# Kernel optimization log

Measured on AMD Instinct MI355X. Metric: run time of the kernel, lower is better.

## Reference

```python
import jax, jax.numpy as jnp
import numpy as np

N = 131072   # octree nodes at this depth
C = 192      # channels (depthwise)
K = 27       # 3x3x3 neighbor stencil
BN_EPS = 1e-5


def setup_inputs() -> dict:
    key = jax.random.key(0)
    k1, k2, k3 = jax.random.split(key, 3)
    data = jax.random.normal(k1, (N, C), dtype=jnp.float32)
    # Octree neighbor table: for each node, indices of its 27 stencil neighbors.
    neigh = jax.random.randint(k2, (N, K), 0, N)
    # Depthwise weights [K, C] (OctreeDWConv, use_bias=False)
    weight = jax.random.normal(k3, (K, C), dtype=jnp.float32) * 0.05
    gamma = jnp.ones((C,), dtype=jnp.float32)
    beta = jnp.zeros((C,), dtype=jnp.float32)
    return {"data": data, "neigh": neigh, "weight": weight,
            "gamma": gamma, "beta": beta}


def reference(data, neigh, weight, gamma, beta):
    # Depthwise octree conv: out[n, c] = sum_k data[neigh[n, k], c] * weight[k, c]
    # Scan over the 27 stencil taps so we never materialize the [N, K, C] gather.
    def step(acc, kin):
        idx_k, w_k = kin          # idx_k: [N], w_k: [C]
        return acc + data[idx_k] * w_k, None

    acc0 = jnp.zeros_like(data)
    out, _ = jax.lax.scan(step, acc0, (neigh.T, weight))  # out: [N, C]

    # BatchNorm1d (training mode: batch statistics over the node dimension)
    mean = jnp.mean(out, axis=0)
    var = jnp.var(out, axis=0)
    return (out - mean) * jax.lax.rsqrt(var + BN_EPS) * gamma + beta
```

## Files before the change

### kernel.cpp

```cpp
#include <hip/hip_runtime.h>


static constexpr int NN = 131072;
static constexpr int CC = 192;
static constexpr int KK = 27;
static constexpr int NB = 32;
static constexpr float BN_EPS = 1e-5f;

typedef float          f32x4 __attribute__((ext_vector_type(4)));
typedef unsigned short u16x4 __attribute__((ext_vector_type(4)));
typedef unsigned int   u32x2 __attribute__((ext_vector_type(2)));

__device__ __forceinline__ unsigned short f2bf_rne(float x) {
    unsigned u = __float_as_uint(x);
    return (unsigned short)((u + 0x7FFFu + ((u >> 16) & 1u)) >> 16);
}

__global__ __launch_bounds__(256) void cvt_zero(
    const float* __restrict__ src, unsigned short* __restrict__ dst,
    float* __restrict__ stats )
{
    if (blockIdx.x < 2 && threadIdx.x < CC)
        stats[blockIdx.x * CC + threadIdx.x] = 0.f;

    const int i = blockIdx.x * 256 + threadIdx.x;
    const f32x4 v =
        __builtin_nontemporal_load(reinterpret_cast<const f32x4*>(src) + i);
    u16x4 o;
    o.x = f2bf_rne(v.x); o.y = f2bf_rne(v.y);
    o.z = f2bf_rne(v.z); o.w = f2bf_rne(v.w);
    reinterpret_cast<u16x4*>(dst)[i] = o;
}

__global__ __launch_bounds__(192, 8) void conv_r4(
    const unsigned short* __restrict__ data_bf,
    const int*   __restrict__ neigh,
    const float* __restrict__ weight,
    unsigned short* __restrict__ conv_bf,
    float*       __restrict__ ch_sum,
    float*       __restrict__ ch_sumsq)
{
    __shared__ float lds_w[KK * CC];

    const int c    = threadIdx.x;
    const int base = blockIdx.x * NB;

#pragma unroll
    for (int k = 0; k < KK; ++k) lds_w[k * CC + c] = weight[k * CC + c];
    __syncthreads();

    float s = 0.f, ss = 0.f;

    for (int n = 0; n < NB; ++n) {
        const int node = base + n;
        const int* nrow = neigh + node * KK;

        unsigned short r[KK];
#pragma unroll
        for (int k = 0; k < KK; ++k)
            r[k] = data_bf[(size_t)nrow[k] * CC + c];

        float acc = 0.f;
#pragma unroll
        for (int k = 0; k < KK; ++k)
            acc = fmaf(__uint_as_float((unsigned)r[k] << 16),
                       lds_w[k * CC + c], acc);

        __builtin_nontemporal_store(f2bf_rne(acc),
                                    &conv_bf[(size_t)node * CC + c]);
        s  += acc;
        ss += acc * acc;
    }

    atomicAdd(&ch_sum[c],   s);
    atomicAdd(&ch_sumsq[c], ss);
}

__global__ __launch_bounds__(192) void bn_apply_fused(
    const unsigned int* __restrict__ conv_bf,
    const float* __restrict__ ch_sum,
    const float* __restrict__ ch_sumsq,
    const float* __restrict__ gamma,
    const float* __restrict__ beta,
    float* __restrict__ out)
{
    const int t = threadIdx.x;
    const int g = t / 48;
    const int q = t - g * 48;
    const int cb = q * 4;

    const float inv_n = 1.0f / (float)NN;
    f32x4 sc, bi;
    {
        float m0 = ch_sum[cb + 0] * inv_n, m1 = ch_sum[cb + 1] * inv_n;
        float m2 = ch_sum[cb + 2] * inv_n, m3 = ch_sum[cb + 3] * inv_n;
        float v0 = ch_sumsq[cb + 0] * inv_n - m0 * m0;
        float v1 = ch_sumsq[cb + 1] * inv_n - m1 * m1;
        float v2 = ch_sumsq[cb + 2] * inv_n - m2 * m2;
        float v3 = ch_sumsq[cb + 3] * inv_n - m3 * m3;
        sc.x = gamma[cb + 0] * rsqrtf(v0 + BN_EPS);
        sc.y = gamma[cb + 1] * rsqrtf(v1 + BN_EPS);
        sc.z = gamma[cb + 2] * rsqrtf(v2 + BN_EPS);
        sc.w = gamma[cb + 3] * rsqrtf(v3 + BN_EPS);
        bi.x = beta[cb + 0] - m0 * sc.x;
        bi.y = beta[cb + 1] - m1 * sc.y;
        bi.z = beta[cb + 2] - m2 * sc.z;
        bi.w = beta[cb + 3] - m3 * sc.w;
    }

    for (int nb = blockIdx.x; nb < NN / 4; nb += gridDim.x) {
        const int node = nb * 4 + g;
        const int i = node * 48 + q;
        const u32x2 u = __builtin_nontemporal_load(
            reinterpret_cast<const u32x2*>(conv_bf) + i);
        f32x4 v;
        v.x = fmaf(__uint_as_float(u.x << 16),         sc.x, bi.x);
        v.y = fmaf(__uint_as_float(u.x & 0xFFFF0000u), sc.y, bi.y);
        v.z = fmaf(__uint_as_float(u.y << 16),         sc.z, bi.z);
        v.w = fmaf(__uint_as_float(u.y & 0xFFFF0000u), sc.w, bi.w);
        __builtin_nontemporal_store(v, reinterpret_cast<f32x4*>(out) + i);
    }
}

__global__ __launch_bounds__(CC) void conv_bn_partial_f32(
    const float* __restrict__ data,
    const int*   __restrict__ neigh,
    const float* __restrict__ weight,
    float*       __restrict__ conv_out,
    float*       __restrict__ ch_sum,
    float*       __restrict__ ch_sumsq)
{
    const int c = threadIdx.x;
    const int base = blockIdx.x * NB;
    float w[KK];
#pragma unroll
    for (int k = 0; k < KK; ++k) w[k] = weight[k * CC + c];
    float s = 0.f, ss = 0.f;
    for (int n = 0; n < NB; ++n) {
        const int node = base + n;
        const int* nrow = neigh + node * KK;
        float acc = 0.f;
#pragma unroll
        for (int k = 0; k < KK; ++k)
            acc = fmaf(data[nrow[k] * CC + c], w[k], acc);
        conv_out[node * CC + c] = acc;
        s += acc; ss += acc * acc;
    }
    atomicAdd(&ch_sum[c], s);
    atomicAdd(&ch_sumsq[c], ss);
}

__global__ __launch_bounds__(192) void bn_apply_f32_fused(
    float* __restrict__ out,
    const float* __restrict__ ch_sum,
    const float* __restrict__ ch_sumsq,
    const float* __restrict__ gamma,
    const float* __restrict__ beta)
{
    const int t = threadIdx.x;
    const int g = t / 48;
    const int q = t - g * 48;
    const int cb = q * 4;
    const float inv_n = 1.0f / (float)NN;
    float4 sc, bi;
    float m0 = ch_sum[cb+0]*inv_n, m1 = ch_sum[cb+1]*inv_n;
    float m2 = ch_sum[cb+2]*inv_n, m3 = ch_sum[cb+3]*inv_n;
    sc.x = gamma[cb+0]*rsqrtf(ch_sumsq[cb+0]*inv_n - m0*m0 + BN_EPS);
    sc.y = gamma[cb+1]*rsqrtf(ch_sumsq[cb+1]*inv_n - m1*m1 + BN_EPS);
    sc.z = gamma[cb+2]*rsqrtf(ch_sumsq[cb+2]*inv_n - m2*m2 + BN_EPS);
    sc.w = gamma[cb+3]*rsqrtf(ch_sumsq[cb+3]*inv_n - m3*m3 + BN_EPS);
    bi.x = beta[cb+0] - m0*sc.x; bi.y = beta[cb+1] - m1*sc.y;
    bi.z = beta[cb+2] - m2*sc.z; bi.w = beta[cb+3] - m3*sc.w;
    for (int nb = blockIdx.x; nb < NN / 4; nb += gridDim.x) {
        const int i = (nb * 4 + g) * 48 + q;
        float4 v = reinterpret_cast<float4*>(out)[i];
        v.x = fmaf(v.x, sc.x, bi.x); v.y = fmaf(v.y, sc.y, bi.y);
        v.z = fmaf(v.z, sc.z, bi.z); v.w = fmaf(v.w, sc.w, bi.w);
        reinterpret_cast<float4*>(out)[i] = v;
    }
}

extern "C" void kernel_launch(void* const* d_in, const int* in_sizes, int n_in,
                              void* d_out, int out_size, void* d_ws, size_t ws_size,
                              hipStream_t stream) {
    const float* data   = (const float*)d_in[0];
    const int*   neigh  = (const int*)  d_in[1];
    const float* weight = (const float*)d_in[2];
    const float* gamma  = (const float*)d_in[3];
    const float* beta   = (const float*)d_in[4];
    float* out = (float*)d_out;

    float* stats    = (float*)d_ws;
    float* ch_sum   = stats;
    float* ch_sumsq = stats + CC;
    unsigned short* data_bf = (unsigned short*)((char*)d_ws + 4096);
    const size_t stage_bytes = (size_t)NN * CC * sizeof(unsigned short);
    unsigned short* conv_bf =
        (unsigned short*)((char*)d_ws + 4096 + stage_bytes);

    const size_t need_full = 4096 + 2 * stage_bytes;
    const int vec_grid = (NN * CC / 4) / 256;

    if (ws_size >= need_full) {
        cvt_zero<<<vec_grid, 256, 0, stream>>>(data, data_bf, stats);
        conv_r4<<<NN / NB, 192, 0, stream>>>(
            data_bf, neigh, weight, conv_bf, ch_sum, ch_sumsq);
        bn_apply_fused<<<8192, 192, 0, stream>>>(
            (const unsigned int*)conv_bf, ch_sum, ch_sumsq, gamma, beta, out);
    } else {
        hipMemsetAsync(stats, 0, 2 * CC * sizeof(float), stream);
        conv_bn_partial_f32<<<NN / NB, CC, 0, stream>>>(
            data, neigh, weight, out, ch_sum, ch_sumsq);
        bn_apply_f32_fused<<<8192, 192, 0, stream>>>(
            out, ch_sum, ch_sumsq, gamma, beta);
    }
}
```

Before: 408.5 us.

## Split bf16 staging into channel-plane layout and run conv in three channel passes

The bf16 conversion now writes data as three planes of 64 channels each, and the convolution runs as three launches, one per 64-channel plane. Each gather then reads 128 bytes per neighbor row, and each pass works on a 16 MB plane that has a better chance of staying in cache, in place of random rows over the full 48 MB array. The conv block now holds 4 wavefronts of 64 channels. Per-block statistics are reduced in shared memory before the atomics. The cost is reading the neighbor table three times and two extra kernel launches.

```diff
diff --git a/kernel.cpp b/kernel.cpp
--- a/kernel.cpp
+++ b/kernel.cpp
@@ -1,10 +1,12 @@
 #include <hip/hip_runtime.h>
 
 
-static constexpr int NN = 131072;
-static constexpr int CC = 192;
-static constexpr int KK = 27;
-static constexpr int NB = 32;
+static constexpr int NN  = 131072;
+static constexpr int CC  = 192;
+static constexpr int KK  = 27;
+static constexpr int CP  = 64;
+static constexpr int NP  = 3;
+static constexpr int NBP = 16;
 static constexpr float BN_EPS = 1e-5f;
 
 typedef float          f32x4 __attribute__((ext_vector_type(4)));
@@ -15,6 +17,9 @@
     unsigned u = __float_as_uint(x);
     return (unsigned short)((u + 0x7FFFu + ((u >> 16) & 1u)) >> 16);
 }
+__device__ __forceinline__ float bf2f(unsigned short b) {
+    return __uint_as_float((unsigned)b << 16);
+}
 
 __global__ __launch_bounds__(256) void cvt_zero(
     const float* __restrict__ src, unsigned short* __restrict__ dst,
@@ -23,57 +28,75 @@
     if (blockIdx.x < 2 && threadIdx.x < CC)
         stats[blockIdx.x * CC + threadIdx.x] = 0.f;
 
-    const int i = blockIdx.x * 256 + threadIdx.x;
+    const int i   = blockIdx.x * 256 + threadIdx.x;
+    const int lin = i * 4;
+    const int n   = lin / CC;
+    const int c   = lin - n * CC;
+    const int p   = c >> 6;
+    const int cr  = c & 63;
+
     const f32x4 v =
         __builtin_nontemporal_load(reinterpret_cast<const f32x4*>(src) + i);
     u16x4 o;
     o.x = f2bf_rne(v.x); o.y = f2bf_rne(v.y);
     o.z = f2bf_rne(v.z); o.w = f2bf_rne(v.w);
-    reinterpret_cast<u16x4*>(dst)[i] = o;
-}
-
-__global__ __launch_bounds__(192, 8) void conv_r4(
-    const unsigned short* __restrict__ data_bf,
+    *reinterpret_cast<u16x4*>(
+        dst + (size_t)p * NN * CP + (size_t)n * CP + cr) = o;
+}
+
+__global__ __launch_bounds__(256, 8) void conv_pass(
+    const unsigned short* __restrict__ dataP,
     const int*   __restrict__ neigh,
     const float* __restrict__ weight,
+    const int pass,
     unsigned short* __restrict__ conv_bf,
     float*       __restrict__ ch_sum,
     float*       __restrict__ ch_sumsq)
 {
-    __shared__ float lds_w[KK * CC];
-
-    const int c    = threadIdx.x;
-    const int base = blockIdx.x * NB;
-
-#pragma unroll
-    for (int k = 0; k < KK; ++k) lds_w[k * CC + c] = weight[k * CC + c];
+    __shared__ float lds_w[KK * CP];
+    __shared__ float red[2][4][CP];
+
+    const int t = threadIdx.x;
+    const int g = t >> 6;
+    const int c = t & 63;
+
+    for (int idx = t; idx < KK * CP; idx += 256)
+        lds_w[idx] = weight[(idx >> 6) * CC + pass * CP + (idx & 63)];
     __syncthreads();
 
+    const int base = (blockIdx.x * 4 + g) * NBP;
+
     float s = 0.f, ss = 0.f;
 
-    for (int n = 0; n < NB; ++n) {
-        const int node = base + n;
-        const int* nrow = neigh + node * KK;
+    for (int n = 0; n < NBP; ++n) {
+        const int node = __builtin_amdgcn_readfirstlane(base + n);
+        const int* nrow = neigh + (size_t)node * KK;
 
         unsigned short r[KK];
 #pragma unroll
         for (int k = 0; k < KK; ++k)
-            r[k] = data_bf[(size_t)nrow[k] * CC + c];
+            r[k] = dataP[(size_t)nrow[k] * CP + c];
 
         float acc = 0.f;
 #pragma unroll
         for (int k = 0; k < KK; ++k)
-            acc = fmaf(__uint_as_float((unsigned)r[k] << 16),
-                       lds_w[k * CC + c], acc);
-
-        __builtin_nontemporal_store(f2bf_rne(acc),
-                                    &conv_bf[(size_t)node * CC + c]);
+            acc = fmaf(bf2f(r[k]), lds_w[k * CP + c], acc);
+
+        __builtin_nontemporal_store(
+            f2bf_rne(acc), &conv_bf[(size_t)node * CC + pass * CP + c]);
         s  += acc;
         ss += acc * acc;
     }
 
-    atomicAdd(&ch_sum[c],   s);
-    atomicAdd(&ch_sumsq[c], ss);
+    red[0][g][c] = s;
+    red[1][g][c] = ss;
+    __syncthreads();
+    if (g == 0) {
+        const float S  = red[0][0][c] + red[0][1][c] + red[0][2][c] + red[0][3][c];
+        const float SS = red[1][0][c] + red[1][1][c] + red[1][2][c] + red[1][3][c];
+        atomicAdd(&ch_sum[pass * CP + c],   S);
+        atomicAdd(&ch_sumsq[pass * CP + c], SS);
+    }
 }
 
 __global__ __launch_bounds__(192) void bn_apply_fused(
@@ -131,12 +154,12 @@
     float*       __restrict__ ch_sumsq)
 {
     const int c = threadIdx.x;
-    const int base = blockIdx.x * NB;
+    const int base = blockIdx.x * 32;
     float w[KK];
 #pragma unroll
     for (int k = 0; k < KK; ++k) w[k] = weight[k * CC + c];
     float s = 0.f, ss = 0.f;
-    for (int n = 0; n < NB; ++n) {
+    for (int n = 0; n < 32; ++n) {
         const int node = base + n;
         const int* nrow = neigh + node * KK;
         float acc = 0.f;
@@ -200,16 +223,19 @@
 
     const size_t need_full = 4096 + 2 * stage_bytes;
     const int vec_grid = (NN * CC / 4) / 256;
+    const int conv_grid = NN / (4 * NBP);
 
     if (ws_size >= need_full) {
         cvt_zero<<<vec_grid, 256, 0, stream>>>(data, data_bf, stats);
-        conv_r4<<<NN / NB, 192, 0, stream>>>(
-            data_bf, neigh, weight, conv_bf, ch_sum, ch_sumsq);
+        for (int p = 0; p < NP; ++p)
+            conv_pass<<<conv_grid, 256, 0, stream>>>(
+                data_bf + (size_t)p * NN * CP, neigh, weight, p,
+                conv_bf, ch_sum, ch_sumsq);
         bn_apply_fused<<<8192, 192, 0, stream>>>(
             (const unsigned int*)conv_bf, ch_sum, ch_sumsq, gamma, beta, out);
     } else {
         hipMemsetAsync(stats, 0, 2 * CC * sizeof(float), stream);
-        conv_bn_partial_f32<<<NN / NB, CC, 0, stream>>>(
+        conv_bn_partial_f32<<<NN / 32, CC, 0, stream>>>(
             data, neigh, weight, out, ch_sum, ch_sumsq);
         bn_apply_f32_fused<<<8192, 192, 0, stream>>>(
             out, ch_sum, ch_sumsq, gamma, beta);
```

New measurement: 492.7 us. +20.6%, slower.
